# Optimization experiments

Hardware: AMD Instinct MI355X
Metric: run time of the kernel (lower is better)

The kernel has to match this reference:

```python
import jax, jax.numpy as jnp
import numpy as np

B, N, S, D_IN, D_OUT = 8, 8192, 8, 64, 64


def setup_inputs() -> dict:
    key = jax.random.key(0)
    ks = jax.random.split(key, 7)
    x = jax.random.normal(ks[0], (B, N, D_IN), dtype=jnp.float32)
    j_idx = jax.random.randint(ks[1], (B, N, S), 0, N, dtype=jnp.int32)
    k_idx = jax.random.randint(ks[2], (B, N, S), 0, N, dtype=jnp.int32)
    # MLP params: Linear(3d -> 2d), GELU, Linear(2d -> d_out)
    s1 = 1.0 / np.sqrt(3 * D_IN)
    s2 = 1.0 / np.sqrt(2 * D_IN)
    W1 = jax.random.uniform(ks[3], (3 * D_IN, 2 * D_IN), jnp.float32, -s1, s1)
    b1 = jax.random.uniform(ks[4], (2 * D_IN,), jnp.float32, -s1, s1)
    W2 = jax.random.uniform(ks[5], (2 * D_IN, D_OUT), jnp.float32, -s2, s2)
    b2 = jax.random.uniform(ks[6], (D_OUT,), jnp.float32, -s2, s2)
    return {"x": x, "j_idx": j_idx, "k_idx": k_idx, "W1": W1, "b1": b1, "W2": W2, "b2": b2}


def reference(x, j_idx, k_idx, W1, b1, W2, b2):
    # x: (B,N,D); j_idx/k_idx: (B,N,S) indices into N
    gather = jax.vmap(lambda xb, ib: xb[ib])  # per-batch gather -> (N,S,D)
    xj = gather(x, j_idx)                      # (B,N,S,D)
    xk = gather(x, k_idx)                      # (B,N,S,D)
    xi = jnp.broadcast_to(x[:, :, None, :], xj.shape)
    triple = jnp.concatenate([xi, xj, xk], axis=-1)  # (B,N,S,3D)
    h = jax.nn.gelu(triple @ W1 + b1, approximate=False)  # (B,N,S,2D)
    out = h @ W2 + b2                                       # (B,N,S,D_OUT)
    return out.mean(axis=2)                                 # (B,N,D_OUT)
```

## Files before the change

kernel.cpp:

```cpp
#include <hip/hip_runtime.h>
#include <stdint.h>


typedef short  short8 __attribute__((ext_vector_type(8)));
typedef float  f32x2  __attribute__((ext_vector_type(2)));
typedef float  f32x4  __attribute__((ext_vector_type(4)));
typedef float  f32x16 __attribute__((ext_vector_type(16)));
typedef _Float16 h16x2 __attribute__((ext_vector_type(2)));
typedef _Float16 h16x4 __attribute__((ext_vector_type(4)));

__device__ __forceinline__ unsigned short f2bf(float f){
  union { float f; unsigned u; } a; a.f = f;
  unsigned u = a.u;
  u += 0x7fffu + ((u >> 16) & 1u);
  return (unsigned short)(u >> 16);
}
__device__ __forceinline__ f32x2 gelu2(f32x2 x){
  f32x2 x2 = x * x;
  f32x2 t  = x2 * (-0.1029437f) + (-2.3022083f);
  f32x2 xt = x * t;
  f32x2 r;
  r[0] = __builtin_amdgcn_rcpf(1.0f + __builtin_amdgcn_exp2f(xt[0]));
  r[1] = __builtin_amdgcn_rcpf(1.0f + __builtin_amdgcn_exp2f(xt[1]));
  return x * r;
}

__global__ void prep_w(const float* __restrict__ W1, const float* __restrict__ W2,
                       short* __restrict__ w1f, short* __restrict__ w2f){
  const int f = blockIdx.x, lane = threadIdx.x;
  short8 v;
  if (f < 48){
    const int cb = f >> 2, t = f & 3;
    #pragma unroll
    for (int j = 0; j < 8; j++)
      v[j] = (short)f2bf(W1[((cb >> 2) * 64 + t * 16 + 8 * (lane >> 5) + j) * 128
                            + (cb & 3) * 32 + (lane & 31)]);
    *(short8*)(w1f + (long)(f * 64 + lane) * 8) = v;
  } else {
    const int g = f - 48, w = g >> 2, q = g & 3;
    #pragma unroll
    for (int j = 0; j < 8; j++)
      v[j] = (short)f2bf(W2[(q * 32 + 8 * (lane >> 4) + j) * 64 + w * 16 + (lane & 15)]);
    *(short8*)(w2f + (long)(g * 64 + lane) * 8) = v;
  }
}

__global__ __launch_bounds__(256, 4) void pgemm(
    const float* __restrict__ x, const short* __restrict__ w1f,
    _Float16* __restrict__ PA, _Float16* __restrict__ PG)
{
  const int tid = threadIdx.x;
  const int w = tid >> 6, lane = tid & 63;
  const int l31 = lane & 31, hi = lane >> 5;
  const int bid = blockIdx.x;
  const int n0 = (bid & 7) * 8192 + (bid >> 3) * 32;

  short8 xf[4];
  #pragma unroll
  for (int t = 0; t < 4; t++){
    const float* xr = x + (long)(n0 + l31) * 64 + t * 16 + 8 * hi;
    float4 a = *(const float4*)xr;
    float4 b = *(const float4*)(xr + 4);
    short8 v;
    v[0]=(short)f2bf(a.x); v[1]=(short)f2bf(a.y); v[2]=(short)f2bf(a.z); v[3]=(short)f2bf(a.w);
    v[4]=(short)f2bf(b.x); v[5]=(short)f2bf(b.y); v[6]=(short)f2bf(b.z); v[7]=(short)f2bf(b.w);
    xf[t] = v;
  }

  #pragma unroll
  for (int ci = 0; ci < 3; ci++){
    const int cb = w * 3 + ci;
    f32x16 acc;
    #pragma unroll
    for (int r = 0; r < 16; r++) acc[r] = 0.f;
    #pragma unroll
    for (int t = 0; t < 4; t++){
      short8 wf = *(const short8*)(w1f + (long)((cb * 4 + t) * 64 + lane) * 8);
      acc = __builtin_amdgcn_mfma_f32_32x32x16_bf16(wf, xf[t], acc, 0, 0, 0);
    }
    _Float16* base = (cb < 4)
        ? (PA + (long)(n0 + l31) * 128 + cb * 32)
        : (PG + (long)(n0 + l31) * 256 + (cb - 4) * 32);
    #pragma unroll
    for (int g = 0; g < 4; g++){
      h16x4 pk;
      pk[0] = (_Float16)acc[4*g+0]; pk[1] = (_Float16)acc[4*g+1];
      pk[2] = (_Float16)acc[4*g+2]; pk[3] = (_Float16)acc[4*g+3];
      *(h16x4*)(base + 8 * g + 4 * hi) = pk;
    }
  }
}

__global__ __launch_bounds__(256, 4) void ltc_main(
    const _Float16* __restrict__ PA, const _Float16* __restrict__ PG,
    const short* __restrict__ w2f,
    const int* __restrict__ jidx,   const int* __restrict__ kidx,
    const float* __restrict__ b1,   const float* __restrict__ b2,
    float* __restrict__ out)
{
  __shared__ short HB[2][16 * 136];

  const int tid  = threadIdx.x;
  const int w    = tid >> 6, lane = tid & 63;
  const int l15  = lane & 15, q4 = lane >> 4;

  short8 w2v[4];
  #pragma unroll
  for (int q = 0; q < 4; q++)
    w2v[q] = *(const short8*)(w2f + (long)((w * 4 + q) * 64 + lane) * 8);
  const float b2v = b2[w * 16 + l15];
  const float2 b1p = *(const float2*)(b1 + lane * 2);

  const int bid   = blockIdx.x;
  const int batch = bid & 7;
  const int gbase = batch * 8192 + (bid >> 3) * 64;
  const unsigned bb = (unsigned)(batch << 13);

  auto gemm2_store = [&](int hb, int ttp){
    f32x4 acc2 = {0.f, 0.f, 0.f, 0.f};
    #pragma unroll
    for (int q2 = 0; q2 < 4; q2++){
      short8 hbf = *(const short8*)((const char*)&HB[hb][0] + l15 * 272 + q2 * 64 + q4 * 16);
      acc2 = __builtin_amdgcn_mfma_f32_16x16x32_bf16(hbf, w2v[q2], acc2, 0, 0, 0);
    }
    long Gn = (long)(gbase + ttp * 16);
    #pragma unroll
    for (int r = 0; r < 4; r++)
      out[(Gn + 4 * q4 + r) * 64 + w * 16 + l15] = acc2[r] + b2v;
  };

  for (int tt = 0; tt < 4; ++tt){
    asm volatile("s_waitcnt lgkmcnt(0)\n\ts_barrier" ::: "memory");
    if (tt > 0) gemm2_store((tt ^ 1) & 1, tt - 1);

    #pragma unroll
    for (int u = 0; u < 4; u++){
      const int nl = w * 4 + u;
      const int gn = gbase + tt * 16 + nl;
      const int4 j0 = *(const int4*)(jidx + (long)gn * 8);
      const int4 j1 = *(const int4*)(jidx + (long)gn * 8 + 4);
      const int4 k0 = *(const int4*)(kidx + (long)gn * 8);
      const int4 k1 = *(const int4*)(kidx + (long)gn * 8 + 4);
      const int jv[8] = {j0.x, j0.y, j0.z, j0.w, j1.x, j1.y, j1.z, j1.w};
      const int kv[8] = {k0.x, k0.y, k0.z, k0.w, k1.x, k1.y, k1.z, k1.w};

      h16x2 av = *(const h16x2*)(PA + (long)gn * 128 + lane * 2);
      f32x2 af; af[0] = (float)av[0] + b1p.x; af[1] = (float)av[1] + b1p.y;

      f32x2 hs = {0.f, 0.f};
      #pragma unroll
      for (int s = 0; s < 8; s++){
        h16x2 v1 = *(const h16x2*)(PG + (long)(bb + (unsigned)jv[s]) * 256 + lane * 2);
        h16x2 v2 = *(const h16x2*)(PG + (long)(bb + (unsigned)kv[s]) * 256 + 128 + lane * 2);
        h16x2 vs = v1 + v2;
        f32x2 z;
        z[0] = af[0] + (float)vs[0];
        z[1] = af[1] + (float)vs[1];
        hs += gelu2(z);
      }
      hs *= 0.125f;
      unsigned pk = (unsigned)f2bf(hs[0]) | ((unsigned)f2bf(hs[1]) << 16);
      *(unsigned*)&HB[tt & 1][nl * 136 + lane * 2] = pk;
    }
  }

  asm volatile("s_waitcnt lgkmcnt(0)\n\ts_barrier" ::: "memory");
  gemm2_store(1, 3);
}

__global__ void ltc_naive(const float* __restrict__ x, const int* __restrict__ jidx,
                          const int* __restrict__ kidx, const float* __restrict__ W1,
                          const float* __restrict__ b1, const float* __restrict__ W2,
                          const float* __restrict__ b2, float* __restrict__ out)
{
  int gidx = blockIdx.x;
  int b = gidx >> 13;
  __shared__ float trip[8][192];
  __shared__ float hb[128];
  int t = threadIdx.x;
  for (int i = t; i < 8 * 192; i += 128){
    int s = i / 192, c = i - s * 192;
    int v = c >> 6, cc = c & 63;
    int src;
    if (v == 0)      src = gidx & 8191;
    else if (v == 1) src = jidx[gidx * 8 + s];
    else             src = kidx[gidx * 8 + s];
    trip[s][c] = x[((long)(b << 13) + src) * 64 + cc];
  }
  __syncthreads();
  float z[8];
  #pragma unroll
  for (int s = 0; s < 8; s++) z[s] = b1[t];
  for (int k = 0; k < 192; k++){
    float wv = W1[k * 128 + t];
    #pragma unroll
    for (int s = 0; s < 8; s++) z[s] = fmaf(trip[s][k], wv, z[s]);
  }
  float acc = 0.f;
  #pragma unroll
  for (int s = 0; s < 8; s++){
    f32x2 zz; zz[0] = z[s]; zz[1] = z[s];
    acc += gelu2(zz)[0];
  }
  hb[t] = acc * 0.125f;
  __syncthreads();
  if (t < 64){
    float o = b2[t];
    for (int h = 0; h < 128; h++) o = fmaf(hb[h], W2[h * 64 + t], o);
    out[(long)gidx * 64 + t] = o;
  }
}

extern "C" void kernel_launch(void* const* d_in, const int* in_sizes, int n_in,
                              void* d_out, int out_size, void* d_ws, size_t ws_size,
                              hipStream_t stream) {
  const float* x   = (const float*)d_in[0];
  const int*   jix = (const int*)  d_in[1];
  const int*   kix = (const int*)  d_in[2];
  const float* W1  = (const float*)d_in[3];
  const float* b1  = (const float*)d_in[4];
  const float* W2  = (const float*)d_in[5];
  const float* b2  = (const float*)d_in[6];
  float* out = (float*)d_out;

  const size_t w1f_elems = 48 * 64 * 8;
  const size_t w2f_elems = 16 * 64 * 8;
  const size_t pa_elems  = (size_t)65536 * 128;
  const size_t pg_elems  = (size_t)65536 * 256;
  const size_t need = (w1f_elems + w2f_elems + pa_elems + pg_elems) * 2;

  if (ws_size >= need){
    short*    w1f = (short*)d_ws;
    short*    w2f = w1f + w1f_elems;
    _Float16* PA  = (_Float16*)(w2f + w2f_elems);
    _Float16* PG  = PA + pa_elems;
    prep_w<<<64, 64, 0, stream>>>(W1, W2, w1f, w2f);
    pgemm<<<2048, 256, 0, stream>>>(x, w1f, PA, PG);
    ltc_main<<<1024, 256, 0, stream>>>(PA, PG, w2f, jix, kix, b1, b2, out);
  } else {
    ltc_naive<<<8 * 8192, 128, 0, stream>>>(x, jix, kix, W1, b1, W2, b2, out);
  }
}
```

Measured before the change: 67.83 us.

## Drop weight-prep kernel, convert weights in-kernel with packed bf16 cvt, nontemporal IO

Removes the separate prep_w launch. pgemm and ltc_main now load W1/W2 directly in fp32 and convert them to bf16 MFMA fragments in registers with v_cvt_pk_bf16_f32. The manual bf16 rounding is replaced by the hardware packed conversion everywhere. Streaming loads and stores of x, PA and out are marked nontemporal so they do not pollute cache. In exchange, every block redundantly performs strided fp32 weight loads, and the one-kernel launch gap goes away.

Result: slower. 87.27 us (+28.7%).

```diff
diff --git a/kernel.cpp b/kernel.cpp
--- a/kernel.cpp
+++ b/kernel.cpp
@@ -9,11 +9,10 @@
 typedef _Float16 h16x2 __attribute__((ext_vector_type(2)));
 typedef _Float16 h16x4 __attribute__((ext_vector_type(4)));
 
-__device__ __forceinline__ unsigned short f2bf(float f){
-  union { float f; unsigned u; } a; a.f = f;
-  unsigned u = a.u;
-  u += 0x7fffu + ((u >> 16) & 1u);
-  return (unsigned short)(u >> 16);
+__device__ __forceinline__ unsigned cvtpk(float lo, float hi){
+  unsigned r;
+  asm("v_cvt_pk_bf16_f32 %0, %1, %2" : "=v"(r) : "v"(lo), "v"(hi));
+  return r;
 }
 __device__ __forceinline__ f32x2 gelu2(f32x2 x){
   f32x2 x2 = x * x;
@@ -25,28 +24,8 @@
   return x * r;
 }
 
-__global__ void prep_w(const float* __restrict__ W1, const float* __restrict__ W2,
-                       short* __restrict__ w1f, short* __restrict__ w2f){
-  const int f = blockIdx.x, lane = threadIdx.x;
-  short8 v;
-  if (f < 48){
-    const int cb = f >> 2, t = f & 3;
-    #pragma unroll
-    for (int j = 0; j < 8; j++)
-      v[j] = (short)f2bf(W1[((cb >> 2) * 64 + t * 16 + 8 * (lane >> 5) + j) * 128
-                            + (cb & 3) * 32 + (lane & 31)]);
-    *(short8*)(w1f + (long)(f * 64 + lane) * 8) = v;
-  } else {
-    const int g = f - 48, w = g >> 2, q = g & 3;
-    #pragma unroll
-    for (int j = 0; j < 8; j++)
-      v[j] = (short)f2bf(W2[(q * 32 + 8 * (lane >> 4) + j) * 64 + w * 16 + (lane & 15)]);
-    *(short8*)(w2f + (long)(g * 64 + lane) * 8) = v;
-  }
-}
-
 __global__ __launch_bounds__(256, 4) void pgemm(
-    const float* __restrict__ x, const short* __restrict__ w1f,
+    const float* __restrict__ x, const float* __restrict__ W1,
     _Float16* __restrict__ PA, _Float16* __restrict__ PG)
 {
   const int tid = threadIdx.x;
@@ -55,16 +34,33 @@
   const int bid = blockIdx.x;
   const int n0 = (bid & 7) * 8192 + (bid >> 3) * 32;
 
+  short8 wfr[3][4];
+  #pragma unroll
+  for (int ci = 0; ci < 3; ci++){
+    const int cb = w * 3 + ci;
+    const int col = (cb & 3) * 32 + l31;
+    #pragma unroll
+    for (int t = 0; t < 4; t++){
+      const int rb = (cb >> 2) * 64 + t * 16 + 8 * hi;
+      const float* wp = W1 + (long)rb * 128 + col;
+      union { unsigned u[4]; short8 s; } cv;
+      #pragma unroll
+      for (int p = 0; p < 4; p++)
+        cv.u[p] = cvtpk(wp[(2*p) * 128], wp[(2*p + 1) * 128]);
+      wfr[ci][t] = cv.s;
+    }
+  }
+
   short8 xf[4];
   #pragma unroll
   for (int t = 0; t < 4; t++){
-    const float* xr = x + (long)(n0 + l31) * 64 + t * 16 + 8 * hi;
-    float4 a = *(const float4*)xr;
-    float4 b = *(const float4*)(xr + 4);
-    short8 v;
-    v[0]=(short)f2bf(a.x); v[1]=(short)f2bf(a.y); v[2]=(short)f2bf(a.z); v[3]=(short)f2bf(a.w);
-    v[4]=(short)f2bf(b.x); v[5]=(short)f2bf(b.y); v[6]=(short)f2bf(b.z); v[7]=(short)f2bf(b.w);
-    xf[t] = v;
+    const f32x4* xr = (const f32x4*)(x + (long)(n0 + l31) * 64 + t * 16 + 8 * hi);
+    f32x4 a = __builtin_nontemporal_load(xr);
+    f32x4 b = __builtin_nontemporal_load(xr + 1);
+    union { unsigned u[4]; short8 s; } cv;
+    cv.u[0] = cvtpk(a[0], a[1]); cv.u[1] = cvtpk(a[2], a[3]);
+    cv.u[2] = cvtpk(b[0], b[1]); cv.u[3] = cvtpk(b[2], b[3]);
+    xf[t] = cv.s;
   }
 
   #pragma unroll
@@ -74,26 +70,28 @@
     #pragma unroll
     for (int r = 0; r < 16; r++) acc[r] = 0.f;
     #pragma unroll
-    for (int t = 0; t < 4; t++){
-      short8 wf = *(const short8*)(w1f + (long)((cb * 4 + t) * 64 + lane) * 8);
-      acc = __builtin_amdgcn_mfma_f32_32x32x16_bf16(wf, xf[t], acc, 0, 0, 0);
-    }
-    _Float16* base = (cb < 4)
-        ? (PA + (long)(n0 + l31) * 128 + cb * 32)
-        : (PG + (long)(n0 + l31) * 256 + (cb - 4) * 32);
+    for (int t = 0; t < 4; t++)
+      acc = __builtin_amdgcn_mfma_f32_32x32x16_bf16(wfr[ci][t], xf[t], acc, 0, 0, 0);
+
     #pragma unroll
     for (int g = 0; g < 4; g++){
       h16x4 pk;
       pk[0] = (_Float16)acc[4*g+0]; pk[1] = (_Float16)acc[4*g+1];
       pk[2] = (_Float16)acc[4*g+2]; pk[3] = (_Float16)acc[4*g+3];
-      *(h16x4*)(base + 8 * g + 4 * hi) = pk;
+      if (cb < 4){
+        h16x4* dst = (h16x4*)(PA + (long)(n0 + l31) * 128 + cb * 32 + 8 * g + 4 * hi);
+        __builtin_nontemporal_store(pk, dst);
+      } else {
+        h16x4* dst = (h16x4*)(PG + (long)(n0 + l31) * 256 + (cb - 4) * 32 + 8 * g + 4 * hi);
+        *dst = pk;
+      }
     }
   }
 }
 
 __global__ __launch_bounds__(256, 4) void ltc_main(
     const _Float16* __restrict__ PA, const _Float16* __restrict__ PG,
-    const short* __restrict__ w2f,
+    const float* __restrict__ W2,
     const int* __restrict__ jidx,   const int* __restrict__ kidx,
     const float* __restrict__ b1,   const float* __restrict__ b2,
     float* __restrict__ out)
@@ -106,8 +104,14 @@
 
   short8 w2v[4];
   #pragma unroll
-  for (int q = 0; q < 4; q++)
-    w2v[q] = *(const short8*)(w2f + (long)((w * 4 + q) * 64 + lane) * 8);
+  for (int q2 = 0; q2 < 4; q2++){
+    const float* wp = W2 + (long)(q2 * 32 + 8 * q4) * 64 + w * 16 + l15;
+    union { unsigned u[4]; short8 s; } cv;
+    #pragma unroll
+    for (int p = 0; p < 4; p++)
+      cv.u[p] = cvtpk(wp[(2*p) * 64], wp[(2*p + 1) * 64]);
+    w2v[q2] = cv.s;
+  }
   const float b2v = b2[w * 16 + l15];
   const float2 b1p = *(const float2*)(b1 + lane * 2);
 
@@ -126,7 +130,8 @@
     long Gn = (long)(gbase + ttp * 16);
     #pragma unroll
     for (int r = 0; r < 4; r++)
-      out[(Gn + 4 * q4 + r) * 64 + w * 16 + l15] = acc2[r] + b2v;
+      __builtin_nontemporal_store(acc2[r] + b2v,
+          &out[(Gn + 4 * q4 + r) * 64 + w * 16 + l15]);
   };
 
   for (int tt = 0; tt < 4; ++tt){
@@ -144,8 +149,9 @@
       const int jv[8] = {j0.x, j0.y, j0.z, j0.w, j1.x, j1.y, j1.z, j1.w};
       const int kv[8] = {k0.x, k0.y, k0.z, k0.w, k1.x, k1.y, k1.z, k1.w};
 
-      h16x2 av = *(const h16x2*)(PA + (long)gn * 128 + lane * 2);
-      f32x2 af; af[0] = (float)av[0] + b1p.x; af[1] = (float)av[1] + b1p.y;
+      union { unsigned u32; h16x2 h; } avu;
+      avu.u32 = __builtin_nontemporal_load((const unsigned*)(PA + (long)gn * 128) + lane);
+      f32x2 af; af[0] = (float)avu.h[0] + b1p.x; af[1] = (float)avu.h[1] + b1p.y;
 
       f32x2 hs = {0.f, 0.f};
       #pragma unroll
@@ -159,8 +165,7 @@
         hs += gelu2(z);
       }
       hs *= 0.125f;
-      unsigned pk = (unsigned)f2bf(hs[0]) | ((unsigned)f2bf(hs[1]) << 16);
-      *(unsigned*)&HB[tt & 1][nl * 136 + lane * 2] = pk;
+      *(unsigned*)&HB[tt & 1][nl * 136 + lane * 2] = cvtpk(hs[0], hs[1]);
     }
   }
 
@@ -223,20 +228,15 @@
   const float* b2  = (const float*)d_in[6];
   float* out = (float*)d_out;
 
-  const size_t w1f_elems = 48 * 64 * 8;
-  const size_t w2f_elems = 16 * 64 * 8;
-  const size_t pa_elems  = (size_t)65536 * 128;
-  const size_t pg_elems  = (size_t)65536 * 256;
-  const size_t need = (w1f_elems + w2f_elems + pa_elems + pg_elems) * 2;
+  const size_t pa_elems = (size_t)65536 * 128;
+  const size_t pg_elems = (size_t)65536 * 256;
+  const size_t need = (pa_elems + pg_elems) * 2;
 
   if (ws_size >= need){
-    short*    w1f = (short*)d_ws;
-    short*    w2f = w1f + w1f_elems;
-    _Float16* PA  = (_Float16*)(w2f + w2f_elems);
-    _Float16* PG  = PA + pa_elems;
-    prep_w<<<64, 64, 0, stream>>>(W1, W2, w1f, w2f);
-    pgemm<<<2048, 256, 0, stream>>>(x, w1f, PA, PG);
-    ltc_main<<<1024, 256, 0, stream>>>(PA, PG, w2f, jix, kix, b1, b2, out);
+    _Float16* PA = (_Float16*)d_ws;
+    _Float16* PG = PA + pa_elems;
+    pgemm<<<2048, 256, 0, stream>>>(x, W1, PA, PG);
+    ltc_main<<<1024, 256, 0, stream>>>(PA, PG, W2, jix, kix, b1, b2, out);
   } else {
     ltc_naive<<<8 * 8192, 128, 0, stream>>>(x, jix, kix, W1, b1, W2, b2, out);
   }
```
